# Optimization experiments

Hardware: AMD Instinct MI355X
Metric: run time of the kernel (lower is better)

Reference implementation:

```python
import jax, jax.numpy as jnp
import numpy as np
from jax import lax

# ---- static config (matches init_kwargs) ----
BATCH, SEQ, D_MODEL = 2, 512, 1024
D_STATE, EXPAND, HEADDIM, D_CONV = 64, 2, 64, 4
VNUM, HORIZON = 3, 20
D_INNER = EXPAND * D_MODEL            # 2048
NHEADS = D_INNER // HEADDIM           # 32
CONV_DIM = D_INNER + 2 * D_STATE      # x, B, C go through the depthwise conv
D_IN_PROJ = 2 * D_INNER + 2 * D_STATE + NHEADS  # z | xBC | dt
RMS_EPS = 1e-5


def setup_inputs() -> dict:
    key = jax.random.key(0)
    ks = jax.random.split(key, 10)
    s = 0.02
    return {
        "embed_data": jax.random.normal(ks[0], (BATCH, SEQ, D_MODEL), jnp.float32),
        "in_proj_w": (jax.random.normal(ks[1], (D_IN_PROJ, D_MODEL), jnp.float32) * s),
        "conv_w": (jax.random.normal(ks[2], (CONV_DIM, D_CONV), jnp.float32) * s),
        "conv_b": jnp.zeros((CONV_DIM,), jnp.float32),
        # dt_bias = softplus^{-1}(dt_init) with dt_init ~ U(1e-3, 0.1), as in Mamba2
        "dt_bias": jnp.log(jnp.expm1(jax.random.uniform(ks[3], (NHEADS,), jnp.float32, 1e-3, 0.1))),
        # A = -exp(A_log), A_init ~ U(1, 16)
        "A_log": jnp.log(jax.random.uniform(ks[4], (NHEADS,), jnp.float32, 1.0, 16.0)),
        "D": jnp.ones((NHEADS,), jnp.float32),
        "norm_w": jnp.ones((D_INNER,), jnp.float32),
        "out_proj_w": (jax.random.normal(ks[5], (D_MODEL, D_INNER), jnp.float32) * s),
        "dec_cur_w": (jax.random.normal(ks[6], (VNUM, D_MODEL), jnp.float32) * s),
        "dec_cur_b": jnp.zeros((VNUM,), jnp.float32),
        "dec_fut_w": (jax.random.normal(ks[7], (HORIZON * VNUM, D_MODEL), jnp.float32) * s),
        "dec_fut_b": jnp.zeros((HORIZON * VNUM,), jnp.float32),
    }


def _mamba2(embed_data, in_proj_w, conv_w, conv_b, dt_bias, A_log, D, norm_w, out_proj_w):
    b, s, _ = embed_data.shape
    zxbcdt = jnp.einsum('bsd,ed->bse', embed_data, in_proj_w)  # [B,S,D_IN_PROJ]
    z = zxbcdt[..., :D_INNER]
    xBC = zxbcdt[..., D_INNER:D_INNER + CONV_DIM]
    dt = zxbcdt[..., D_INNER + CONV_DIM:]                      # [B,S,H]

    # causal depthwise conv1d (kernel=4) + silu
    xpad = jnp.pad(xBC, ((0, 0), (D_CONV - 1, 0), (0, 0)))
    xBC = sum(conv_w[:, k] * xpad[:, k:k + s, :] for k in range(D_CONV)) + conv_b
    xBC = jax.nn.silu(xBC)

    x = xBC[..., :D_INNER].reshape(b, s, NHEADS, HEADDIM)       # [B,S,H,P]
    Bm = xBC[..., D_INNER:D_INNER + D_STATE]                    # [B,S,N]
    Cm = xBC[..., D_INNER + D_STATE:]                           # [B,S,N]

    dt = jax.nn.softplus(dt + dt_bias)                          # [B,S,H]
    A = -jnp.exp(A_log)                                         # [H]

    # selective state-space scan: h_t = exp(dt*A) h_{t-1} + dt * x_t B_t^T
    def step(h, inp):
        x_t, dt_t, b_t, c_t = inp                               # [B,H,P],[B,H],[B,N],[B,N]
        dA = jnp.exp(dt_t * A)                                  # [B,H]
        h = h * dA[..., None, None] + (dt_t[..., None] * x_t)[..., None] * b_t[:, None, None, :]
        y = jnp.einsum('bhpn,bn->bhp', h, c_t)
        return h, y

    h0 = jnp.zeros((b, NHEADS, HEADDIM, D_STATE), embed_data.dtype)
    xs = (x.transpose(1, 0, 2, 3), dt.transpose(1, 0, 2),
          Bm.transpose(1, 0, 2), Cm.transpose(1, 0, 2))
    _, ys = lax.scan(step, h0, xs)                              # [S,B,H,P]
    y = ys.transpose(1, 0, 2, 3) + D[None, None, :, None] * x   # skip term D*x
    y = y.reshape(b, s, D_INNER)

    # gated RMSNorm: rmsnorm(y * silu(z)) * w
    y = y * jax.nn.silu(z)
    y = y * lax.rsqrt(jnp.mean(y * y, axis=-1, keepdims=True) + RMS_EPS) * norm_w
    return jnp.einsum('bsi,di->bsd', y, out_proj_w)             # [B,S,D_MODEL]


def reference(embed_data, in_proj_w, conv_w, conv_b, dt_bias, A_log, D, norm_w,
              out_proj_w, dec_cur_w, dec_cur_b, dec_fut_w, dec_fut_b):
    h = _mamba2(embed_data, in_proj_w, conv_w, conv_b, dt_bias, A_log, D, norm_w, out_proj_w)
    pred_current = jnp.einsum('bsd,vd->bsv', h, dec_cur_w) + dec_cur_b         # [B,S,V]
    pred_future = (h[:, -1] @ dec_fut_w.T + dec_fut_b).reshape(h.shape[0], HORIZON, VNUM)
    return (pred_current, pred_future)
```

## Files before the change

### kernel.cpp

```cpp
#include <hip/hip_runtime.h>
#include <hip/hip_bf16.h>

#define BATCH   2
#define SEQ     512
#define DMODEL  1024
#define DSTATE  64
#define HEADDIM 64
#define DCONV   4
#define VNUM    3
#define HORIZON 20
#define DINNER  2048
#define NHEADS  32
#define CONVDIM 2176
#define DINPROJ 4256
#define NPAD1   4352
#define BS      (BATCH*SEQ)
#define RMS_EPS 1e-5f
#define CHUNK   64
#define NCHUNK  (SEQ/CHUNK)

typedef __attribute__((ext_vector_type(8))) short bf16x8;
typedef __attribute__((ext_vector_type(4))) float f32x4;

__device__ __forceinline__ unsigned short f2b(float x) {
    union { float f; unsigned u; } v; v.f = x;
    return (unsigned short)((v.u + 0x7fffu + ((v.u >> 16) & 1u)) >> 16);
}

__device__ __forceinline__ void async16(const void* g, const void* l) {
    __builtin_amdgcn_global_load_lds(
        (const __attribute__((address_space(1))) unsigned int*)g,
        (__attribute__((address_space(3))) unsigned int*)l, 16, 0, 0);
}

template<int BM, int BN, int FM, int FN, int KD>
__global__ __launch_bounds__(256) void gemm_bf16(const short* __restrict__ A,
                                                 const short* __restrict__ B,
                                                 float* __restrict__ C, int N) {
    constexpr int WM = FM * 16, WN = FN * 16;
    static_assert(BM == 2 * WM && BN == 2 * WN, "2x2 waves");
    __shared__ __align__(16) short At[BM * 32];
    __shared__ __align__(16) short Bt[BN * 32];
    const int t    = threadIdx.x;
    const int lane = t & 63;
    const int w    = t >> 6;
    const int wm   = (w >> 1) * WM, wn = (w & 1) * WN;
    const int row0 = blockIdx.y * BM, col0 = blockIdx.x * BN;
    const int fr   = lane & 15;
    const int kq   = lane >> 4;
    const int lr   = t >> 2;
    const int lc   = (t & 3) * 8;

    const short* Ag = A + (size_t)(row0 + lr) * KD + lc;
    const short* Bg = B + (size_t)(col0 + lr) * KD + lc;

    f32x4 acc[FM][FN];
#pragma unroll
    for (int i = 0; i < FM; ++i)
#pragma unroll
        for (int j = 0; j < FN; ++j)
#pragma unroll
            for (int r = 0; r < 4; ++r) acc[i][j][r] = 0.f;

    for (int k0 = 0; k0 < KD; k0 += 32) {
        __syncthreads();
#pragma unroll
        for (int i = 0; i < BM / 64; ++i)
            async16(Ag + (size_t)i * 64 * KD + k0, (const char*)At + i * 4096 + t * 16);
#pragma unroll
        for (int i = 0; i < BN / 64; ++i)
            async16(Bg + (size_t)i * 64 * KD + k0, (const char*)Bt + i * 4096 + t * 16);
        __syncthreads();

        bf16x8 af[FM], bv[FN];
#pragma unroll
        for (int i = 0; i < FM; ++i)
            af[i] = *(const bf16x8*)&At[(wm + i * 16 + fr) * 32 + kq * 8];
#pragma unroll
        for (int j = 0; j < FN; ++j)
            bv[j] = *(const bf16x8*)&Bt[(wn + j * 16 + fr) * 32 + kq * 8];
#pragma unroll
        for (int i = 0; i < FM; ++i)
#pragma unroll
            for (int j = 0; j < FN; ++j)
                acc[i][j] = __builtin_amdgcn_mfma_f32_16x16x32_bf16(
                    af[i], bv[j], acc[i][j], 0, 0, 0);
    }

    const int orow = lane >> 4;
#pragma unroll
    for (int i = 0; i < FM; ++i)
#pragma unroll
        for (int j = 0; j < FN; ++j) {
            const int col = col0 + wn + j * 16 + fr;
            if (col < N) {
#pragma unroll
                for (int r = 0; r < 4; ++r) {
                    const int row = row0 + wm + i * 16 + orow * 4 + r;
                    C[(size_t)row * N + col] = acc[i][j][r];
                }
            }
        }
}

__global__ __launch_bounds__(256) void cast_bf16_kernel(const float* __restrict__ in,
                                                        short* __restrict__ out, int n4) {
    const int i = blockIdx.x * 256 + threadIdx.x;
    if (i >= n4) return;
    float4 v = *(const float4*)(in + (size_t)i * 4);
    short4 o = make_short4((short)f2b(v.x), (short)f2b(v.y),
                           (short)f2b(v.z), (short)f2b(v.w));
    *(short4*)(out + (size_t)i * 4) = o;
}

__global__ __launch_bounds__(256) void cast_pad_kernel(const float* __restrict__ in,
                                                       short* __restrict__ out) {
    const int i = blockIdx.x * 256 + threadIdx.x;
    const size_t e0 = (size_t)i * 4;
    const int row = (int)(e0 / DMODEL);
    short4 o;
    if (row < DINPROJ) {
        float4 v = *(const float4*)(in + e0);
        o = make_short4((short)f2b(v.x), (short)f2b(v.y),
                        (short)f2b(v.z), (short)f2b(v.w));
    } else {
        o = make_short4(0, 0, 0, 0);
    }
    *(short4*)(out + e0) = o;
}

__global__ __launch_bounds__(256) void conv_silu_kernel(
        const float* __restrict__ zxbcdt, const float* __restrict__ cw,
        const float* __restrict__ cb, float* __restrict__ xbc) {
    const int idx = blockIdx.x * 256 + threadIdx.x;
    if (idx >= BS * CONVDIM) return;
    const int c  = idx % CONVDIM;
    const int rs = idx / CONVDIM;
    const int s  = rs % SEQ;
    const float* src = zxbcdt + (size_t)rs * DINPROJ + DINNER + c;
    float acc = cb[c];
    const float w0 = cw[c * 4 + 0], w1 = cw[c * 4 + 1];
    const float w2 = cw[c * 4 + 2], w3 = cw[c * 4 + 3];
    if (s >= 3) acc += w0 * src[-3 * DINPROJ];
    if (s >= 2) acc += w1 * src[-2 * DINPROJ];
    if (s >= 1) acc += w2 * src[-1 * DINPROJ];
    acc += w3 * src[0];
    acc = acc / (1.f + expf(-acc));
    xbc[(size_t)rs * CONVDIM + c] = acc;
}

__global__ __launch_bounds__(256) void dt_softplus_kernel(
        const float* __restrict__ zxbcdt, const float* __restrict__ dt_bias,
        float* __restrict__ dts) {
    const int idx = blockIdx.x * 256 + threadIdx.x;
    if (idx >= BS * NHEADS) return;
    const int h  = idx % NHEADS;
    const int rs = idx / NHEADS;
    const float v = zxbcdt[(size_t)rs * DINPROJ + DINNER + CONVDIM + h] + dt_bias[h];
    const float sp = fmaxf(v, 0.f) + log1pf(expf(-fabsf(v)));
    dts[idx] = sp;
}

__global__ __launch_bounds__(256) void chunk_intra_kernel(
        const float* __restrict__ xbc, const float* __restrict__ dts,
        const float* __restrict__ A_log, const float* __restrict__ Dv,
        float* __restrict__ yraw, float* __restrict__ Sc,
        float* __restrict__ dexp) {
    const int blk = blockIdx.x;
    const int c  = blk & 7;
    const int bh = blk >> 3;
    const int h  = bh & 31;
    const int b  = bh >> 5;
    const int rs0 = b * SEQ + c * CHUNK;

    __shared__ float sBn[64][68];
    __shared__ float sX [64][68];
    __shared__ float sMT[64][68];
    __shared__ float sl[64], se[64], sdt[64];

    const int tid = threadIdx.x;
    const float A = -expf(A_log[h]);

    {
        const int row = tid >> 2;
        const int cq  = tid & 3;
        const float* xrow = xbc + (size_t)(rs0 + row) * CONVDIM;
#pragma unroll
        for (int i = 0; i < 4; ++i) {
            const int n = cq * 16 + i * 4;
            float4 bv = *(const float4*)(xrow + DINNER + n);
            float4 cv = *(const float4*)(xrow + DINNER + DSTATE + n);
            sBn[n+0][row] = bv.x; sBn[n+1][row] = bv.y;
            sBn[n+2][row] = bv.z; sBn[n+3][row] = bv.w;
            sX [n+0][row] = cv.x; sX [n+1][row] = cv.y;
            sX [n+2][row] = cv.z; sX [n+3][row] = cv.w;
        }
    }

    if (tid < 64) {
        const float dtv = dts[(size_t)(rs0 + tid) * NHEADS + h];
        sdt[tid] = dtv;
        float v = dtv * A;
#pragma unroll
        for (int off = 1; off < 64; off <<= 1) {
            float o = __shfl_up(v, off, 64);
            if (tid >= off) v += o;
        }
        sl[tid] = v;
        const float ltot = __shfl(v, 63, 64);
        se[tid] = expf(ltot - v);
        dexp[(size_t)blk * 64 + tid] = expf(v);
    }
    __syncthreads();

    const int g0 = (tid >> 4) * 4;
    const int g1 = (tid & 15) * 4;

    {
        const int t0 = g0, s0 = g1;
        float acc[4][4] = {};
        for (int n = 0; n < 64; ++n) {
            float4 ct = *(const float4*)&sX [n][t0];
            float4 bs = *(const float4*)&sBn[n][s0];
            float cta[4] = {ct.x, ct.y, ct.z, ct.w};
            float bsa[4] = {bs.x, bs.y, bs.z, bs.w};
#pragma unroll
            for (int i = 0; i < 4; ++i)
#pragma unroll
                for (int j = 0; j < 4; ++j) acc[i][j] += cta[i] * bsa[j];
        }
#pragma unroll
        for (int i = 0; i < 4; ++i) {
            const int t = t0 + i;
            const float lt = sl[t];
#pragma unroll
            for (int j = 0; j < 4; ++j) {
                const int s = s0 + j;
                sMT[s][t] = (s <= t) ? expf(lt - sl[s]) * acc[i][j] : 0.f;
            }
        }
    }
    __syncthreads();

    {
        const int row = tid >> 2;
        const int cq  = tid & 3;
        const float* xrow = xbc + (size_t)(rs0 + row) * CONVDIM + h * HEADDIM;
        const float dtv = sdt[row];
#pragma unroll
        for (int i = 0; i < 4; ++i) {
            const int p = cq * 16 + i * 4;
            float4 xv = *(const float4*)(xrow + p);
            sX[row][p+0] = dtv * xv.x; sX[row][p+1] = dtv * xv.y;
            sX[row][p+2] = dtv * xv.z; sX[row][p+3] = dtv * xv.w;
        }
    }
    __syncthreads();

    {
        const int t0 = g0, p0 = g1;
        float acc[4][4] = {};
        for (int s = 0; s < 64; ++s) {
            float4 mt = *(const float4*)&sMT[s][t0];
            float4 us = *(const float4*)&sX [s][p0];
            float mta[4] = {mt.x, mt.y, mt.z, mt.w};
            float usa[4] = {us.x, us.y, us.z, us.w};
#pragma unroll
            for (int i = 0; i < 4; ++i)
#pragma unroll
                for (int j = 0; j < 4; ++j) acc[i][j] += mta[i] * usa[j];
        }
        const float Dh = Dv[h];
#pragma unroll
        for (int i = 0; i < 4; ++i) {
            const int t = t0 + i;
            float4 xv = *(const float4*)(xbc + (size_t)(rs0 + t) * CONVDIM
                                         + h * HEADDIM + p0);
            float4 yv = make_float4(acc[i][0] + Dh * xv.x, acc[i][1] + Dh * xv.y,
                                    acc[i][2] + Dh * xv.z, acc[i][3] + Dh * xv.w);
            *(float4*)&yraw[(size_t)(rs0 + t) * DINNER + h * HEADDIM + p0] = yv;
        }
    }

    {
        const int p0 = g0, n0 = g1;
        float acc[4][4] = {};
        for (int s = 0; s < 64; ++s) {
            const float es = se[s];
            float4 up = *(const float4*)&sX[s][p0];
            float upa[4] = {es * up.x, es * up.y, es * up.z, es * up.w};
            float bna[4] = {sBn[n0+0][s], sBn[n0+1][s], sBn[n0+2][s], sBn[n0+3][s]};
#pragma unroll
            for (int i = 0; i < 4; ++i)
#pragma unroll
                for (int j = 0; j < 4; ++j) acc[i][j] += upa[i] * bna[j];
        }
        float* scp = Sc + (size_t)blk * (HEADDIM * DSTATE);
#pragma unroll
        for (int i = 0; i < 4; ++i) {
            float4 v = make_float4(acc[i][0], acc[i][1], acc[i][2], acc[i][3]);
            *(float4*)&scp[(size_t)(p0 + i) * DSTATE + n0] = v;
        }
    }
}

__global__ __launch_bounds__(256) void state_combine_kernel(
        const float* __restrict__ Sc, const float* __restrict__ dexp,
        float* __restrict__ h0ws) {
    const int bh  = blockIdx.x;
    const int tid = threadIdx.x;
    float hreg[16];
#pragma unroll
    for (int k = 0; k < 16; ++k) hreg[k] = 0.f;
    for (int c = 0; c < NCHUNK; ++c) {
        const size_t base = (size_t)(bh * NCHUNK + c) * (HEADDIM * DSTATE);
        const float ac = dexp[(size_t)(bh * NCHUNK + c) * 64 + 63];
#pragma unroll
        for (int k = 0; k < 16; ++k) {
            const int e = tid + k * 256;
            h0ws[base + e] = hreg[k];
            hreg[k] = ac * hreg[k] + Sc[base + e];
        }
    }
}

__global__ __launch_bounds__(256) void chunk_state_out_kernel(
        const float* __restrict__ xbc, const float* __restrict__ h0ws,
        const float* __restrict__ dexp, float* __restrict__ yraw) {
    const int blk = blockIdx.x;
    const int c  = blk & 7;
    if (c == 0) return;
    const int bh = blk >> 3;
    const int h  = bh & 31;
    const int b  = bh >> 5;
    const int rs0 = b * SEQ + c * CHUNK;

    __shared__ float sCn[64][68];
    __shared__ float sH [64][68];
    __shared__ float sdex[64];
    const int tid = threadIdx.x;
    {
        const int row = tid >> 2;
        const int cq  = tid & 3;
        const float* xrow = xbc + (size_t)(rs0 + row) * CONVDIM + DINNER + DSTATE;
        const float* hrow = h0ws + (size_t)blk * (HEADDIM * DSTATE) + (size_t)row * DSTATE;
#pragma unroll
        for (int i = 0; i < 4; ++i) {
            const int n = cq * 16 + i * 4;
            float4 cv = *(const float4*)(xrow + n);
            float4 hv = *(const float4*)(hrow + n);
            sCn[n+0][row] = cv.x; sCn[n+1][row] = cv.y;
            sCn[n+2][row] = cv.z; sCn[n+3][row] = cv.w;
            sH [n+0][row] = hv.x; sH [n+1][row] = hv.y;
            sH [n+2][row] = hv.z; sH [n+3][row] = hv.w;
        }
    }
    if (tid < 64) sdex[tid] = dexp[(size_t)blk * 64 + tid];
    __syncthreads();

    const int t0 = (tid >> 4) * 4;
    const int p0 = (tid & 15) * 4;
    float acc[4][4] = {};
    for (int n = 0; n < 64; ++n) {
        float4 ct = *(const float4*)&sCn[n][t0];
        float4 hp = *(const float4*)&sH [n][p0];
        float cta[4] = {ct.x, ct.y, ct.z, ct.w};
        float hpa[4] = {hp.x, hp.y, hp.z, hp.w};
#pragma unroll
        for (int i = 0; i < 4; ++i)
#pragma unroll
            for (int j = 0; j < 4; ++j) acc[i][j] += cta[i] * hpa[j];
    }
#pragma unroll
    for (int i = 0; i < 4; ++i) {
        const float d = sdex[t0 + i];
        float* yp = &yraw[(size_t)(rs0 + t0 + i) * DINNER + h * HEADDIM + p0];
        float4 old = *(const float4*)yp;
        *(float4*)yp = make_float4(old.x + d * acc[i][0], old.y + d * acc[i][1],
                                   old.z + d * acc[i][2], old.w + d * acc[i][3]);
    }
}

__global__ __launch_bounds__(256) void gate_norm_kernel(
        const float* __restrict__ zxbcdt, const float* __restrict__ y,
        short* __restrict__ yb, const float* __restrict__ nw) {
    const int rs = blockIdx.x;
    const int t  = threadIdx.x;
    const float* z = zxbcdt + (size_t)rs * DINPROJ;
    const float* yr = y + (size_t)rs * DINNER;
    short* yo = yb + (size_t)rs * DINNER;

    float vals[8];
    float ss = 0.f;
#pragma unroll
    for (int i = 0; i < 8; ++i) {
        const int c = t + i * 256;
        const float zv = z[c];
        const float v  = yr[c] * (zv / (1.f + expf(-zv)));
        vals[i] = v;
        ss += v * v;
    }
#pragma unroll
    for (int off = 32; off > 0; off >>= 1) ss += __shfl_down(ss, off, 64);
    __shared__ float red[4];
    if ((t & 63) == 0) red[t >> 6] = ss;
    __syncthreads();
    const float tot   = red[0] + red[1] + red[2] + red[3];
    const float scale = rsqrtf(tot / (float)DINNER + RMS_EPS);
#pragma unroll
    for (int i = 0; i < 8; ++i) {
        const int c = t + i * 256;
        yo[c] = (short)f2b(vals[i] * scale * nw[c]);
    }
}

__global__ __launch_bounds__(256) void pred_cur_kernel(
        const float* __restrict__ hout, const float* __restrict__ w,
        const float* __restrict__ bvec, float* __restrict__ out) {
    const int rs = blockIdx.x;
    const int t  = threadIdx.x;
    const float* hr = hout + (size_t)rs * DMODEL;
    float p0 = 0.f, p1 = 0.f, p2 = 0.f;
    for (int i = t; i < DMODEL; i += 256) {
        const float hv = hr[i];
        p0 += hv * w[i];
        p1 += hv * w[DMODEL + i];
        p2 += hv * w[2 * DMODEL + i];
    }
#pragma unroll
    for (int off = 32; off > 0; off >>= 1) {
        p0 += __shfl_down(p0, off, 64);
        p1 += __shfl_down(p1, off, 64);
        p2 += __shfl_down(p2, off, 64);
    }
    __shared__ float red[4][3];
    if ((t & 63) == 0) {
        red[t >> 6][0] = p0; red[t >> 6][1] = p1; red[t >> 6][2] = p2;
    }
    __syncthreads();
    if (t < 3) {
        const float s = red[0][t] + red[1][t] + red[2][t] + red[3][t];
        out[(size_t)rs * VNUM + t] = s + bvec[t];
    }
}

__global__ __launch_bounds__(256) void pred_fut_kernel(
        const float* __restrict__ hout, const float* __restrict__ w,
        const float* __restrict__ bvec, float* __restrict__ out) {
    const int blk = blockIdx.x;
    const int b = blk / (HORIZON * VNUM);
    const int j = blk % (HORIZON * VNUM);
    const float* hr = hout + ((size_t)b * SEQ + (SEQ - 1)) * DMODEL;
    const float* wr = w + (size_t)j * DMODEL;
    float pv = 0.f;
    for (int i = threadIdx.x; i < DMODEL; i += 256) pv += hr[i] * wr[i];
#pragma unroll
    for (int off = 32; off > 0; off >>= 1) pv += __shfl_down(pv, off, 64);
    __shared__ float red[4];
    if ((threadIdx.x & 63) == 0) red[threadIdx.x >> 6] = pv;
    __syncthreads();
    if (threadIdx.x == 0)
        out[b * (HORIZON * VNUM) + j] = red[0] + red[1] + red[2] + red[3] + bvec[j];
}

extern "C" void kernel_launch(void* const* d_in, const int* in_sizes, int n_in,
                              void* d_out, int out_size, void* d_ws, size_t ws_size,
                              hipStream_t stream) {
    const float* embed      = (const float*)d_in[0];
    const float* in_proj_w  = (const float*)d_in[1];
    const float* conv_w     = (const float*)d_in[2];
    const float* conv_b     = (const float*)d_in[3];
    const float* dt_bias    = (const float*)d_in[4];
    const float* A_log      = (const float*)d_in[5];
    const float* Dv         = (const float*)d_in[6];
    const float* norm_w     = (const float*)d_in[7];
    const float* out_proj_w = (const float*)d_in[8];
    const float* dec_cur_w  = (const float*)d_in[9];
    const float* dec_cur_b  = (const float*)d_in[10];
    const float* dec_fut_w  = (const float*)d_in[11];
    const float* dec_fut_b  = (const float*)d_in[12];

    float* ws     = (float*)d_ws;
    float* zxbcdt = ws;
    float* xbc    = zxbcdt + (size_t)BS * DINPROJ;
    float* dts    = xbc    + (size_t)BS * CONVDIM;
    float* yraw   = dts    + (size_t)BS * NHEADS;
    float* hout   = yraw   + (size_t)BS * DINNER;
    float* Sc     = hout   + (size_t)BS * DMODEL;
    float* h0ws   = Sc     + (size_t)BATCH*NHEADS*NCHUNK*HEADDIM*DSTATE;
    float* dexp   = h0ws   + (size_t)BATCH*NHEADS*NCHUNK*HEADDIM*DSTATE;
    short* embB   = (short*)(dexp + (size_t)BATCH*NHEADS*NCHUNK*64);
    short* ipwB   = embB + (size_t)BS * DMODEL;
    short* opwB   = ipwB + (size_t)NPAD1 * DMODEL;
    short* ybB    = opwB + (size_t)DMODEL * DINNER;

    float* out = (float*)d_out;

    cast_bf16_kernel<<<(BS * DMODEL / 4 + 255) / 256, 256, 0, stream>>>(
        embed, embB, BS * DMODEL / 4);
    cast_pad_kernel<<<NPAD1 * DMODEL / 4 / 256, 256, 0, stream>>>(in_proj_w, ipwB);
    cast_bf16_kernel<<<(DMODEL * DINNER / 4 + 255) / 256, 256, 0, stream>>>(
        out_proj_w, opwB, DMODEL * DINNER / 4);

    gemm_bf16<128, 128, 4, 4, DMODEL>
        <<<dim3(NPAD1 / 128, BS / 128), 256, 0, stream>>>(embB, ipwB, zxbcdt, DINPROJ);

    conv_silu_kernel<<<(BS * CONVDIM + 255) / 256, 256, 0, stream>>>(zxbcdt, conv_w, conv_b, xbc);
    dt_softplus_kernel<<<(BS * NHEADS + 255) / 256, 256, 0, stream>>>(zxbcdt, dt_bias, dts);

    chunk_intra_kernel<<<BATCH * NHEADS * NCHUNK, 256, 0, stream>>>(
        xbc, dts, A_log, Dv, yraw, Sc, dexp);
    state_combine_kernel<<<BATCH * NHEADS, 256, 0, stream>>>(Sc, dexp, h0ws);
    chunk_state_out_kernel<<<BATCH * NHEADS * NCHUNK, 256, 0, stream>>>(
        xbc, h0ws, dexp, yraw);

    gate_norm_kernel<<<BS, 256, 0, stream>>>(zxbcdt, yraw, ybB, norm_w);

    gemm_bf16<64, 64, 2, 2, DINNER>
        <<<dim3(DMODEL / 64, BS / 64), 256, 0, stream>>>(ybB, opwB, hout, DMODEL);

    pred_cur_kernel<<<BS, 256, 0, stream>>>(hout, dec_cur_w, dec_cur_b, out);
    pred_fut_kernel<<<BATCH * HORIZON * VNUM, 256, 0, stream>>>(hout, dec_fut_w, dec_fut_b,
                                                                out + BS * VNUM);
}
```

Before: 208.3 us.

## Fold out_proj into decoder weights, fuse cast and conv/dt kernels

The change precomputes the product of the decoder weights and out_proj_w (63x2048) on every call. This removes the out_proj GEMM, its bf16 casts and the hout buffer, and the gated-norm kernel now computes pred_current directly and saves the last-step normalized row for pred_future. It also fuses the two input cast kernels and the conv/dt kernels (the conv part now vectorized with float4), and retiles the in_proj GEMM to 128x64. The weight-combination step runs in fp32 and adds a small partial-reduce pass, while the GEMM over 2048x1024 weights goes away.

```diff
diff --git a/kernel.cpp b/kernel.cpp
--- a/kernel.cpp
+++ b/kernel.cpp
@@ -18,6 +18,7 @@
 #define RMS_EPS 1e-5f
 #define CHUNK   64
 #define NCHUNK  (SEQ/CHUNK)
+#define NDEC    (VNUM + HORIZON*VNUM)
 
 typedef __attribute__((ext_vector_type(8))) short bf16x8;
 typedef __attribute__((ext_vector_type(4))) float f32x4;
@@ -103,62 +104,111 @@
         }
 }
 
-__global__ __launch_bounds__(256) void cast_bf16_kernel(const float* __restrict__ in,
-                                                        short* __restrict__ out, int n4) {
+#define EMB4  (BS * DMODEL / 4)
+#define IPW4  (NPAD1 * DMODEL / 4)
+__global__ __launch_bounds__(256) void cast_fused_kernel(
+        const float* __restrict__ embed, const float* __restrict__ ipw,
+        short* __restrict__ embB, short* __restrict__ ipwB) {
     const int i = blockIdx.x * 256 + threadIdx.x;
-    if (i >= n4) return;
-    float4 v = *(const float4*)(in + (size_t)i * 4);
-    short4 o = make_short4((short)f2b(v.x), (short)f2b(v.y),
-                           (short)f2b(v.z), (short)f2b(v.w));
-    *(short4*)(out + (size_t)i * 4) = o;
-}
-
-__global__ __launch_bounds__(256) void cast_pad_kernel(const float* __restrict__ in,
-                                                       short* __restrict__ out) {
-    const int i = blockIdx.x * 256 + threadIdx.x;
-    const size_t e0 = (size_t)i * 4;
-    const int row = (int)(e0 / DMODEL);
-    short4 o;
-    if (row < DINPROJ) {
-        float4 v = *(const float4*)(in + e0);
-        o = make_short4((short)f2b(v.x), (short)f2b(v.y),
+    if (i < EMB4) {
+        float4 v = *(const float4*)(embed + (size_t)i * 4);
+        *(short4*)(embB + (size_t)i * 4) =
+            make_short4((short)f2b(v.x), (short)f2b(v.y),
                         (short)f2b(v.z), (short)f2b(v.w));
     } else {
-        o = make_short4(0, 0, 0, 0);
-    }
-    *(short4*)(out + e0) = o;
-}
-
-__global__ __launch_bounds__(256) void conv_silu_kernel(
+        const int j = i - EMB4;
+        const size_t e0 = (size_t)j * 4;
+        const int row = (int)(e0 / DMODEL);
+        short4 o;
+        if (row < DINPROJ) {
+            float4 v = *(const float4*)(ipw + e0);
+            o = make_short4((short)f2b(v.x), (short)f2b(v.y),
+                            (short)f2b(v.z), (short)f2b(v.w));
+        } else {
+            o = make_short4(0, 0, 0, 0);
+        }
+        *(short4*)(ipwB + e0) = o;
+    }
+}
+
+__global__ __launch_bounds__(256) void wcomb_partial_kernel(
+        const float* __restrict__ op, const float* __restrict__ cw,
+        const float* __restrict__ fw, float* __restrict__ P) {
+    const int itile = blockIdx.x & 7;
+    const int ds    = blockIdx.x >> 3;
+    const int i     = itile * 256 + threadIdx.x;
+    const int d0    = ds * 64;
+    float opc[64];
+#pragma unroll
+    for (int d = 0; d < 64; ++d) opc[d] = op[(size_t)(d0 + d) * DINNER + i];
+    for (int v = 0; v < NDEC; ++v) {
+        const float* wr = (v < VNUM) ? (cw + (size_t)v * DMODEL + d0)
+                                     : (fw + (size_t)(v - VNUM) * DMODEL + d0);
+        float a = 0.f;
+#pragma unroll
+        for (int d = 0; d < 64; ++d) a += wr[d] * opc[d];
+        P[((size_t)ds * NDEC + v) * DINNER + i] = a;
+    }
+}
+
+__global__ __launch_bounds__(256) void wcomb_reduce_kernel(
+        const float* __restrict__ P, float* __restrict__ W) {
+    const int idx = blockIdx.x * 256 + threadIdx.x;
+    float s = 0.f;
+#pragma unroll
+    for (int ds = 0; ds < 16; ++ds) s += P[(size_t)ds * NDEC * DINNER + idx];
+    W[idx] = s;
+}
+
+#define CONVBLKS (BS * CONVDIM / 4 / 256)
+__global__ __launch_bounds__(256) void conv_dt_kernel(
         const float* __restrict__ zxbcdt, const float* __restrict__ cw,
-        const float* __restrict__ cb, float* __restrict__ xbc) {
-    const int idx = blockIdx.x * 256 + threadIdx.x;
-    if (idx >= BS * CONVDIM) return;
-    const int c  = idx % CONVDIM;
-    const int rs = idx / CONVDIM;
-    const int s  = rs % SEQ;
-    const float* src = zxbcdt + (size_t)rs * DINPROJ + DINNER + c;
-    float acc = cb[c];
-    const float w0 = cw[c * 4 + 0], w1 = cw[c * 4 + 1];
-    const float w2 = cw[c * 4 + 2], w3 = cw[c * 4 + 3];
-    if (s >= 3) acc += w0 * src[-3 * DINPROJ];
-    if (s >= 2) acc += w1 * src[-2 * DINPROJ];
-    if (s >= 1) acc += w2 * src[-1 * DINPROJ];
-    acc += w3 * src[0];
-    acc = acc / (1.f + expf(-acc));
-    xbc[(size_t)rs * CONVDIM + c] = acc;
-}
-
-__global__ __launch_bounds__(256) void dt_softplus_kernel(
-        const float* __restrict__ zxbcdt, const float* __restrict__ dt_bias,
-        float* __restrict__ dts) {
-    const int idx = blockIdx.x * 256 + threadIdx.x;
-    if (idx >= BS * NHEADS) return;
-    const int h  = idx % NHEADS;
-    const int rs = idx / NHEADS;
-    const float v = zxbcdt[(size_t)rs * DINPROJ + DINNER + CONVDIM + h] + dt_bias[h];
-    const float sp = fmaxf(v, 0.f) + log1pf(expf(-fabsf(v)));
-    dts[idx] = sp;
+        const float* __restrict__ cb, const float* __restrict__ dt_bias,
+        float* __restrict__ xbc, float* __restrict__ dts) {
+    if (blockIdx.x < CONVBLKS) {
+        const int item = blockIdx.x * 256 + threadIdx.x;
+        const int c4 = item % (CONVDIM / 4);
+        const int rs = item / (CONVDIM / 4);
+        const int s  = rs % SEQ;
+        const int c  = c4 * 4;
+        const float* src = zxbcdt + (size_t)rs * DINPROJ + DINNER + c;
+        float4 x0 = (s >= 3) ? *(const float4*)(src - 3 * DINPROJ) : make_float4(0,0,0,0);
+        float4 x1 = (s >= 2) ? *(const float4*)(src - 2 * DINPROJ) : make_float4(0,0,0,0);
+        float4 x2 = (s >= 1) ? *(const float4*)(src - 1 * DINPROJ) : make_float4(0,0,0,0);
+        float4 x3 = *(const float4*)(src);
+        float4 bias = *(const float4*)(cb + c);
+        float4 r;
+        {
+            float4 w = *(const float4*)(cw + (size_t)(c+0)*4);
+            r.x = bias.x + w.x*x0.x + w.y*x1.x + w.z*x2.x + w.w*x3.x;
+        }
+        {
+            float4 w = *(const float4*)(cw + (size_t)(c+1)*4);
+            r.y = bias.y + w.x*x0.y + w.y*x1.y + w.z*x2.y + w.w*x3.y;
+        }
+        {
+            float4 w = *(const float4*)(cw + (size_t)(c+2)*4);
+            r.z = bias.z + w.x*x0.z + w.y*x1.z + w.z*x2.z + w.w*x3.z;
+        }
+        {
+            float4 w = *(const float4*)(cw + (size_t)(c+3)*4);
+            r.w = bias.w + w.x*x0.w + w.y*x1.w + w.z*x2.w + w.w*x3.w;
+        }
+        r.x = r.x / (1.f + expf(-r.x));
+        r.y = r.y / (1.f + expf(-r.y));
+        r.z = r.z / (1.f + expf(-r.z));
+        r.w = r.w / (1.f + expf(-r.w));
+        *(float4*)(xbc + (size_t)rs * CONVDIM + c) = r;
+    } else {
+        const int idx = (blockIdx.x - CONVBLKS) * 256 + threadIdx.x;
+        if (idx < BS * NHEADS) {
+            const int h  = idx % NHEADS;
+            const int rs = idx / NHEADS;
+            const float v = zxbcdt[(size_t)rs * DINPROJ + DINNER + CONVDIM + h]
+                            + dt_bias[h];
+            dts[idx] = fmaxf(v, 0.f) + log1pf(expf(-fabsf(v)));
+        }
+    }
 }
 
 __global__ __launch_bounds__(256) void chunk_intra_kernel(
@@ -381,14 +431,15 @@
     }
 }
 
-__global__ __launch_bounds__(256) void gate_norm_kernel(
+__global__ __launch_bounds__(256) void gate_norm_pred_kernel(
         const float* __restrict__ zxbcdt, const float* __restrict__ y,
-        short* __restrict__ yb, const float* __restrict__ nw) {
+        const float* __restrict__ nw, const float* __restrict__ W,
+        const float* __restrict__ cur_b, float* __restrict__ out,
+        float* __restrict__ ylast) {
     const int rs = blockIdx.x;
     const int t  = threadIdx.x;
-    const float* z = zxbcdt + (size_t)rs * DINPROJ;
+    const float* z  = zxbcdt + (size_t)rs * DINPROJ;
     const float* yr = y + (size_t)rs * DINNER;
-    short* yo = yb + (size_t)rs * DINNER;
 
     float vals[8];
     float ss = 0.f;
@@ -407,25 +458,22 @@
     __syncthreads();
     const float tot   = red[0] + red[1] + red[2] + red[3];
     const float scale = rsqrtf(tot / (float)DINNER + RMS_EPS);
+
+    const bool is_last = ((rs & (SEQ - 1)) == SEQ - 1);
+    float p0 = 0.f, p1 = 0.f, p2 = 0.f;
 #pragma unroll
     for (int i = 0; i < 8; ++i) {
         const int c = t + i * 256;
-        yo[c] = (short)f2b(vals[i] * scale * nw[c]);
-    }
-}
-
-__global__ __launch_bounds__(256) void pred_cur_kernel(
-        const float* __restrict__ hout, const float* __restrict__ w,
-        const float* __restrict__ bvec, float* __restrict__ out) {
-    const int rs = blockIdx.x;
-    const int t  = threadIdx.x;
-    const float* hr = hout + (size_t)rs * DMODEL;
-    float p0 = 0.f, p1 = 0.f, p2 = 0.f;
-    for (int i = t; i < DMODEL; i += 256) {
-        const float hv = hr[i];
-        p0 += hv * w[i];
-        p1 += hv * w[DMODEL + i];
-        p2 += hv * w[2 * DMODEL + i];
+        const float vn = vals[i] * scale * nw[c];
+        vals[i] = vn;
+        p0 += vn * W[c];
+        p1 += vn * W[DINNER + c];
+        p2 += vn * W[2 * DINNER + c];
+    }
+    if (is_last) {
+        float* yl = ylast + (size_t)(rs >> 9) * DINNER;
+#pragma unroll
+        for (int i = 0; i < 8; ++i) yl[t + i * 256] = vals[i];
     }
 #pragma unroll
     for (int off = 32; off > 0; off >>= 1) {
@@ -433,27 +481,25 @@
         p1 += __shfl_down(p1, off, 64);
         p2 += __shfl_down(p2, off, 64);
     }
-    __shared__ float red[4][3];
-    if ((t & 63) == 0) {
-        red[t >> 6][0] = p0; red[t >> 6][1] = p1; red[t >> 6][2] = p2;
-    }
-    __syncthreads();
-    if (t < 3) {
-        const float s = red[0][t] + red[1][t] + red[2][t] + red[3][t];
-        out[(size_t)rs * VNUM + t] = s + bvec[t];
+    __shared__ float r3[4][3];
+    if ((t & 63) == 0) { r3[t >> 6][0] = p0; r3[t >> 6][1] = p1; r3[t >> 6][2] = p2; }
+    __syncthreads();
+    if (t < VNUM) {
+        const float s = r3[0][t] + r3[1][t] + r3[2][t] + r3[3][t];
+        out[(size_t)rs * VNUM + t] = s + cur_b[t];
     }
 }
 
 __global__ __launch_bounds__(256) void pred_fut_kernel(
-        const float* __restrict__ hout, const float* __restrict__ w,
+        const float* __restrict__ ylast, const float* __restrict__ W,
         const float* __restrict__ bvec, float* __restrict__ out) {
     const int blk = blockIdx.x;
     const int b = blk / (HORIZON * VNUM);
     const int j = blk % (HORIZON * VNUM);
-    const float* hr = hout + ((size_t)b * SEQ + (SEQ - 1)) * DMODEL;
-    const float* wr = w + (size_t)j * DMODEL;
+    const float* yl = ylast + (size_t)b * DINNER;
+    const float* wr = W + (size_t)(VNUM + j) * DINNER;
     float pv = 0.f;
-    for (int i = threadIdx.x; i < DMODEL; i += 256) pv += hr[i] * wr[i];
+    for (int i = threadIdx.x; i < DINNER; i += 256) pv += yl[i] * wr[i];
 #pragma unroll
     for (int off = 32; off > 0; off >>= 1) pv += __shfl_down(pv, off, 64);
     __shared__ float red[4];
@@ -485,28 +531,26 @@
     float* xbc    = zxbcdt + (size_t)BS * DINPROJ;
     float* dts    = xbc    + (size_t)BS * CONVDIM;
     float* yraw   = dts    + (size_t)BS * NHEADS;
-    float* hout   = yraw   + (size_t)BS * DINNER;
-    float* Sc     = hout   + (size_t)BS * DMODEL;
+    float* Sc     = yraw   + (size_t)BS * DINNER;
     float* h0ws   = Sc     + (size_t)BATCH*NHEADS*NCHUNK*HEADDIM*DSTATE;
     float* dexp   = h0ws   + (size_t)BATCH*NHEADS*NCHUNK*HEADDIM*DSTATE;
-    short* embB   = (short*)(dexp + (size_t)BATCH*NHEADS*NCHUNK*64);
+    float* Wp     = dexp   + (size_t)BATCH*NHEADS*NCHUNK*64;
+    float* W      = Wp     + (size_t)16 * NDEC * DINNER;
+    float* ylast  = W      + (size_t)NDEC * DINNER;
+    short* embB   = (short*)(ylast + (size_t)BATCH * DINNER);
     short* ipwB   = embB + (size_t)BS * DMODEL;
-    short* opwB   = ipwB + (size_t)NPAD1 * DMODEL;
-    short* ybB    = opwB + (size_t)DMODEL * DINNER;
 
     float* out = (float*)d_out;
 
-    cast_bf16_kernel<<<(BS * DMODEL / 4 + 255) / 256, 256, 0, stream>>>(
-        embed, embB, BS * DMODEL / 4);
-    cast_pad_kernel<<<NPAD1 * DMODEL / 4 / 256, 256, 0, stream>>>(in_proj_w, ipwB);
-    cast_bf16_kernel<<<(DMODEL * DINNER / 4 + 255) / 256, 256, 0, stream>>>(
-        out_proj_w, opwB, DMODEL * DINNER / 4);
-
-    gemm_bf16<128, 128, 4, 4, DMODEL>
-        <<<dim3(NPAD1 / 128, BS / 128), 256, 0, stream>>>(embB, ipwB, zxbcdt, DINPROJ);
-
-    conv_silu_kernel<<<(BS * CONVDIM + 255) / 256, 256, 0, stream>>>(zxbcdt, conv_w, conv_b, xbc);
-    dt_softplus_kernel<<<(BS * NHEADS + 255) / 256, 256, 0, stream>>>(zxbcdt, dt_bias, dts);
+    wcomb_partial_kernel<<<128, 256, 0, stream>>>(out_proj_w, dec_cur_w, dec_fut_w, Wp);
+    wcomb_reduce_kernel<<<NDEC * DINNER / 256, 256, 0, stream>>>(Wp, W);
+
+    cast_fused_kernel<<<(EMB4 + IPW4) / 256, 256, 0, stream>>>(embed, in_proj_w, embB, ipwB);
+    gemm_bf16<128, 64, 4, 2, DMODEL>
+        <<<dim3(NPAD1 / 64, BS / 128), 256, 0, stream>>>(embB, ipwB, zxbcdt, DINPROJ);
+
+    conv_dt_kernel<<<CONVBLKS + (BS * NHEADS + 255) / 256, 256, 0, stream>>>(
+        zxbcdt, conv_w, conv_b, dt_bias, xbc, dts);
 
     chunk_intra_kernel<<<BATCH * NHEADS * NCHUNK, 256, 0, stream>>>(
         xbc, dts, A_log, Dv, yraw, Sc, dexp);
@@ -514,12 +558,9 @@
     chunk_state_out_kernel<<<BATCH * NHEADS * NCHUNK, 256, 0, stream>>>(
         xbc, h0ws, dexp, yraw);
 
-    gate_norm_kernel<<<BS, 256, 0, stream>>>(zxbcdt, yraw, ybB, norm_w);
-
-    gemm_bf16<64, 64, 2, 2, DINNER>
-        <<<dim3(DMODEL / 64, BS / 64), 256, 0, stream>>>(ybB, opwB, hout, DMODEL);
-
-    pred_cur_kernel<<<BS, 256, 0, stream>>>(hout, dec_cur_w, dec_cur_b, out);
-    pred_fut_kernel<<<BATCH * HORIZON * VNUM, 256, 0, stream>>>(hout, dec_fut_w, dec_fut_b,
+    gate_norm_pred_kernel<<<BS, 256, 0, stream>>>(zxbcdt, yraw, norm_w, W,
+                                                  dec_cur_b, out, ylast);
+
+    pred_fut_kernel<<<BATCH * HORIZON * VNUM, 256, 0, stream>>>(ylast, W, dec_fut_b,
                                                                 out + BS * VNUM);
 }
```

After: 223.8 us. 7.4% more time.
